# Performance work log

Measured on AMD Instinct MI355X. Metric: run time of the kernel, lower is better.

## Reference

```python
import jax, jax.numpy as jnp
import numpy as np

B, H, L, D = 2, 16, 2048, 64


def setup_inputs() -> dict:
    key = jax.random.key(0)
    kq, kk, kv = jax.random.split(key, 3)
    q = jax.random.normal(kq, (B, H, L, D), dtype=jnp.float32)
    k = jax.random.normal(kk, (B, H, L, D), dtype=jnp.float32)
    v = jax.random.normal(kv, (B, H, L, D), dtype=jnp.float32)
    return {"q": q, "k": k, "v": v}


def reference(q, k, v):
    use_norm = True
    seq_len = q.shape[-2]
    scale = q.shape[-1] ** (-0.5)
    q = q * scale
    # [B, H, L, L] score matrix
    attn = jnp.einsum("bhqd,bhkd->bhqk", q, k)
    # 2nd-order Taylor expansion of exp: 1 + s + 0.5*s^2
    attn = 1.0 + attn + 0.5 * attn * attn
    # causal mask (lower-triangular kept)
    causal = jnp.tril(jnp.ones((seq_len, seq_len), dtype=bool))
    attn = jnp.where(causal, attn, 0.0)
    o = jnp.einsum("bhqk,bhkd->bhqd", attn, v)
    if use_norm:
        z = attn.sum(-1)
        o = o / (z[..., None] + 1e-06)
    return o
```

## Files before the change

### kernel.cpp

```cpp
#include <hip/hip_runtime.h>
#include <hip/hip_bf16.h>

typedef __bf16    bf16x8  __attribute__((ext_vector_type(8)));
typedef __bf16    bf16x4  __attribute__((ext_vector_type(4)));
typedef _Float16  half8   __attribute__((ext_vector_type(8)));
typedef _Float16  half4   __attribute__((ext_vector_type(4)));
typedef _Float16  half2   __attribute__((ext_vector_type(2)));
typedef float     floatx4 __attribute__((ext_vector_type(4)));

constexpr int Bc  = 2;
constexpr int Hc  = 16;
constexpr int Lc  = 2048;
constexpr int Dc  = 64;
constexpr int BHn = Bc * Hc;
constexpr int BM  = 128;
constexpr int BN  = 128;
constexpr int NQT = Lc / BM;
constexpr int LDK = 72;
constexpr int LDV = 136;

static __device__ __forceinline__ half2 pack_f16(float a, float b) {
    return __builtin_bit_cast(half2, __builtin_amdgcn_cvt_pkrtz(a, b));
}

__global__ void prep(const float* __restrict__ kp, const float* __restrict__ vp,
                     __bf16* __restrict__ k16, _Float16* __restrict__ v16) {
    const int bid = blockIdx.x, tid = threadIdx.x;
    if (bid < 1024) {
        const size_t base = (size_t)bid * 4096 + tid * 4;
        #pragma unroll
        for (int rep = 0; rep < 4; ++rep) {
            const size_t i = base + rep * 1024;
            floatx4 v = *(const floatx4*)(kp + i);
            bf16x4 b;
            b[0] = (__bf16)v[0]; b[1] = (__bf16)v[1]; b[2] = (__bf16)v[2]; b[3] = (__bf16)v[3];
            *(bf16x4*)(k16 + i) = b;
        }
    } else {
        const int vb  = bid - 1024;
        const int bh  = vb >> 5, kt = vb & 31;
        const int key = kt * 64 + (tid & 63);
        const int k5  = key & 31;
        const int pcol = (key & ~31) | (((k5 >> 2) & 3) * 8 + ((k5 >> 4) & 1) * 4 + (k5 & 3));
        const int d0  = (tid >> 6) * 16;
        const float* src = vp + ((size_t)bh * Lc + key) * Dc;
        _Float16*    dst = v16 + (size_t)bh * Dc * Lc + pcol;
        #pragma unroll
        for (int i = 0; i < 16; ++i) {
            const int d = d0 + i;
            dst[(size_t)d * Lc] = (_Float16)src[d];
        }
    }
}

__global__ __launch_bounds__(256, 2)
void taylor_attn(const float* __restrict__ qp, const __bf16* __restrict__ k16,
                 const _Float16* __restrict__ v16, float* __restrict__ op)
{
    __shared__ __bf16   Ks[BN * LDK];
    __shared__ _Float16 VT[Dc * LDV];

    const int tid  = threadIdx.x;
    const int wv   = tid >> 6;
    const int lane = tid & 63;
    const int lm   = lane & 15;
    const int quad = lane >> 4;

    const int cu    = (int)(blockIdx.x & 255);
    const int snd   = (int)(blockIdx.x >> 8);
    const int bh    = cu & 31;
    const int qslot = cu >> 5;
    const int qi    = snd ? qslot : (NQT - 1 - qslot);
    const int q0    = qi * BM;
    const int jmax  = qi;

    const float*    qbase = qp  + ((size_t)bh * Lc + q0) * Dc;
    const __bf16*   kj    = k16 + (size_t)bh * Lc * Dc;
    const _Float16* vj    = v16 + (size_t)bh * Dc * Lc;

    bf16x8 kr[4]; half8 vr[4];
    #pragma unroll
    for (int rep = 0; rep < 4; ++rep)
        kr[rep] = *(const bf16x8*)(kj + 8 * (tid + 256 * rep));
    #pragma unroll
    for (int rep = 0; rep < 4; ++rep) {
        const int g = tid + 256 * rep;
        vr[rep] = *(const half8*)(vj + (size_t)(g >> 4) * Lc + (g & 15) * 8);
    }

    {
        const int r0 = tid >> 4, c4 = tid & 15;
        #pragma unroll
        for (int rep = 0; rep < 8; ++rep) {
            const int row = r0 + rep * 16;
            floatx4 v = *(const floatx4*)(qbase + row * Dc + c4 * 4);
            bf16x4 b;
            b[0] = (__bf16)v[0]; b[1] = (__bf16)v[1]; b[2] = (__bf16)v[2]; b[3] = (__bf16)v[3];
            *(bf16x4*)&Ks[row * LDK + c4 * 4] = b;
        }
    }
    __syncthreads();
    bf16x8 qa[2][2];
    #pragma unroll
    for (int st = 0; st < 2; ++st)
        #pragma unroll
        for (int kf = 0; kf < 2; ++kf)
            qa[st][kf] = *(const bf16x8*)&Ks[(32 * wv + 16 * st + lm) * LDK + kf * 32 + quad * 8];
    __syncthreads();

    floatx4 oacc[2][4] = {};
    floatx4 zacc[2]    = {};

    const half8 ones = {(_Float16)1.f, (_Float16)1.f, (_Float16)1.f, (_Float16)1.f,
                        (_Float16)1.f, (_Float16)1.f, (_Float16)1.f, (_Float16)1.f};
    const half2 c8  = {(_Float16)0.125f, (_Float16)0.125f};
    const half2 c1  = {(_Float16)1.f,    (_Float16)1.f};
    const half2 ch  = {(_Float16)0.5f,   (_Float16)0.5f};

    for (int j = 0; j <= jmax; ++j) {
        #pragma unroll
        for (int rep = 0; rep < 4; ++rep) {
            const int c = tid + 256 * rep;
            *(bf16x8*)&Ks[(c >> 3) * LDK + (c & 7) * 8] = kr[rep];
        }
        #pragma unroll
        for (int rep = 0; rep < 4; ++rep) {
            const int g = tid + 256 * rep;
            *(half8*)&VT[(g >> 4) * LDV + (g & 15) * 8] = vr[rep];
        }
        __syncthreads();

        if (j < jmax) {
            kj += BN * Dc;
            vj += BN;
            #pragma unroll
            for (int rep = 0; rep < 4; ++rep)
                kr[rep] = *(const bf16x8*)(kj + 8 * (tid + 256 * rep));
            #pragma unroll
            for (int rep = 0; rep < 4; ++rep) {
                const int g = tid + 256 * rep;
                vr[rep] = *(const half8*)(vj + (size_t)(g >> 4) * Lc + (g & 15) * 8);
            }
        }

        const bool nm = (j == jmax);
        #pragma unroll
        for (int half = 0; half < 2; ++half) {
            floatx4 sacc[2][4] = {};
            #pragma unroll
            for (int kb4 = 0; kb4 < 4; ++kb4) {
                const int kb = 4 * half + kb4;
                #pragma unroll
                for (int kf = 0; kf < 2; ++kf) {
                    bf16x8 ka = *(const bf16x8*)&Ks[(16 * kb + lm) * LDK + kf * 32 + quad * 8];
                    sacc[0][kb4] = __builtin_amdgcn_mfma_f32_16x16x32_bf16(ka, qa[0][kf], sacc[0][kb4], 0, 0, 0);
                    sacc[1][kb4] = __builtin_amdgcn_mfma_f32_16x16x32_bf16(ka, qa[1][kf], sacc[1][kb4], 0, 0, 0);
                }
            }

            half8 wf[2][2];
            #pragma unroll
            for (int st = 0; st < 2; ++st) {
                const int strip_lo = q0 + 32 * wv + 16 * st;
                const int thr = strip_lo + lm - j * BN;
                half2 wh[4][2];
                #pragma unroll
                for (int kb4 = 0; kb4 < 4; ++kb4) {
                    half2 s01 = pack_f16(sacc[st][kb4][0], sacc[st][kb4][1]);
                    half2 s23 = pack_f16(sacc[st][kb4][2], sacc[st][kb4][3]);
                    half2 a01 = s01 * c8 + c1;
                    half2 a23 = s23 * c8 + c1;
                    half2 w01 = a01 * (a01 * ch) + ch;
                    half2 w23 = a23 * (a23 * ch) + ch;
                    if (nm) {
                        const int i0 = 16 * (4 * half + kb4) + 4 * quad;
                        w01[0] = (i0 + 0 <= thr) ? w01[0] : (_Float16)0.f;
                        w01[1] = (i0 + 1 <= thr) ? w01[1] : (_Float16)0.f;
                        w23[0] = (i0 + 2 <= thr) ? w23[0] : (_Float16)0.f;
                        w23[1] = (i0 + 3 <= thr) ? w23[1] : (_Float16)0.f;
                    }
                    wh[kb4][0] = w01;
                    wh[kb4][1] = w23;
                }
                #pragma unroll
                for (int g2 = 0; g2 < 2; ++g2) {
                    half4 lo = __builtin_shufflevector(wh[2 * g2][0],     wh[2 * g2][1],     0, 1, 2, 3);
                    half4 hi = __builtin_shufflevector(wh[2 * g2 + 1][0], wh[2 * g2 + 1][1], 0, 1, 2, 3);
                    wf[st][g2] = __builtin_shufflevector(lo, hi, 0, 1, 2, 3, 4, 5, 6, 7);
                }
            }

            #pragma unroll
            for (int db = 0; db < 4; ++db)
                #pragma unroll
                for (int g2 = 0; g2 < 2; ++g2) {
                    const int grp = 2 * half + g2;
                    half8 va = *(const half8*)&VT[(16 * db + lm) * LDV + 32 * grp + 8 * quad];
                    oacc[0][db] = __builtin_amdgcn_mfma_f32_16x16x32_f16(va, wf[0][g2], oacc[0][db], 0, 0, 0);
                    oacc[1][db] = __builtin_amdgcn_mfma_f32_16x16x32_f16(va, wf[1][g2], oacc[1][db], 0, 0, 0);
                }
            #pragma unroll
            for (int g2 = 0; g2 < 2; ++g2) {
                zacc[0] = __builtin_amdgcn_mfma_f32_16x16x32_f16(ones, wf[0][g2], zacc[0], 0, 0, 0);
                zacc[1] = __builtin_amdgcn_mfma_f32_16x16x32_f16(ones, wf[1][g2], zacc[1], 0, 0, 0);
            }
        }
        __syncthreads();
    }

    #pragma unroll
    for (int st = 0; st < 2; ++st) {
        const float inv = 1.0f / (zacc[st][0] + 1e-6f);
        const int qrow = q0 + 32 * wv + 16 * st + lm;
        float* orow = op + ((size_t)bh * Lc + qrow) * Dc;
        #pragma unroll
        for (int db = 0; db < 4; ++db)
            #pragma unroll
            for (int r = 0; r < 4; ++r)
                orow[16 * db + 4 * quad + r] = oacc[st][db][r] * inv;
    }
}

extern "C" void kernel_launch(void* const* d_in, const int* in_sizes, int n_in,
                              void* d_out, int out_size, void* d_ws, size_t ws_size,
                              hipStream_t stream) {
    const float* q = (const float*)d_in[0];
    const float* k = (const float*)d_in[1];
    const float* v = (const float*)d_in[2];
    float* o = (float*)d_out;

    __bf16*   k16 = (__bf16*)d_ws;
    _Float16* v16 = (_Float16*)((char*)d_ws + (size_t)BHn * Lc * Dc * 2);

    prep<<<dim3(2048), dim3(256), 0, stream>>>(k, v, k16, v16);
    taylor_attn<<<dim3(NQT * BHn), dim3(256), 0, stream>>>(q, k16, v16, o);
}
```

Baseline: 119.2 us.

## Split each query tile's KV range across two blocks with atomic-flag reduction

Each query tile's causal KV loop is split into two halves handled by separate blocks, doubling the grid to 1024 blocks and rebalancing work so long diagonal tiles no longer dominate the tail. The block that finishes first writes partial O and z to workspace and sets a release flag. The second block spins on the flag, adds the partials and normalizes. Launch bounds are raised to 4 blocks per CU to fit the larger grid. The change adds workspace traffic and a spin-wait, which risks deadlock if the partner block cannot be co-resident.

```diff
diff --git a/kernel.cpp b/kernel.cpp
--- a/kernel.cpp
+++ b/kernel.cpp
@@ -24,8 +24,13 @@
 }
 
 __global__ void prep(const float* __restrict__ kp, const float* __restrict__ vp,
-                     __bf16* __restrict__ k16, _Float16* __restrict__ v16) {
+                     __bf16* __restrict__ k16, _Float16* __restrict__ v16,
+                     int* __restrict__ ctrflag) {
     const int bid = blockIdx.x, tid = threadIdx.x;
+    if (bid == 0 && tid < 256) {
+        #pragma unroll
+        for (int r = 0; r < 4; ++r) ctrflag[tid + 256 * r] = 0;
+    }
     if (bid < 1024) {
         const size_t base = (size_t)bid * 4096 + tid * 4;
         #pragma unroll
@@ -53,12 +58,15 @@
     }
 }
 
-__global__ __launch_bounds__(256, 2)
+__global__ __launch_bounds__(256, 4)
 void taylor_attn(const float* __restrict__ qp, const __bf16* __restrict__ k16,
-                 const _Float16* __restrict__ v16, float* __restrict__ op)
+                 const _Float16* __restrict__ v16, float* __restrict__ op,
+                 float* __restrict__ Oa, float* __restrict__ za,
+                 int* __restrict__ ctr, int* __restrict__ flag)
 {
     __shared__ __bf16   Ks[BN * LDK];
     __shared__ _Float16 VT[Dc * LDV];
+    __shared__ int      s_old;
 
     const int tid  = threadIdx.x;
     const int wv   = tid >> 6;
@@ -66,17 +74,20 @@
     const int lm   = lane & 15;
     const int quad = lane >> 4;
 
-    const int cu    = (int)(blockIdx.x & 255);
-    const int snd   = (int)(blockIdx.x >> 8);
-    const int bh    = cu & 31;
-    const int qslot = cu >> 5;
-    const int qi    = snd ? qslot : (NQT - 1 - qslot);
-    const int q0    = qi * BM;
-    const int jmax  = qi;
+    const int r    = (int)(blockIdx.x >> 8);
+    const int s    = (int)((blockIdx.x >> 5) & 7);
+    const int bh   = (int)(blockIdx.x & 31);
+    const int seff = (r & 1) ? (7 - s) : s;
+    const int qi   = (15 - 4 * r) - (seff >> 1);
+    const int half = seff & 1;
+    const int q0   = qi * BM;
+    const int nlo  = (qi + 2) >> 1;
+    const int j0   = half ? nlo : 0;
+    const int jend = half ? (qi + 1) : nlo;
 
     const float*    qbase = qp  + ((size_t)bh * Lc + q0) * Dc;
-    const __bf16*   kj    = k16 + (size_t)bh * Lc * Dc;
-    const _Float16* vj    = v16 + (size_t)bh * Dc * Lc;
+    const __bf16*   kj    = k16 + (size_t)bh * Lc * Dc + (size_t)j0 * BN * Dc;
+    const _Float16* vj    = v16 + (size_t)bh * Dc * Lc + (size_t)j0 * BN;
 
     bf16x8 kr[4]; half8 vr[4];
     #pragma unroll
@@ -117,7 +128,7 @@
     const half2 c1  = {(_Float16)1.f,    (_Float16)1.f};
     const half2 ch  = {(_Float16)0.5f,   (_Float16)0.5f};
 
-    for (int j = 0; j <= jmax; ++j) {
+    for (int j = j0; j < jend; ++j) {
         #pragma unroll
         for (int rep = 0; rep < 4; ++rep) {
             const int c = tid + 256 * rep;
@@ -130,7 +141,7 @@
         }
         __syncthreads();
 
-        if (j < jmax) {
+        if (j + 1 < jend) {
             kj += BN * Dc;
             vj += BN;
             #pragma unroll
@@ -143,13 +154,13 @@
             }
         }
 
-        const bool nm = (j == jmax);
-        #pragma unroll
-        for (int half = 0; half < 2; ++half) {
+        const bool nm = (j == qi);
+        #pragma unroll
+        for (int kh = 0; kh < 2; ++kh) {
             floatx4 sacc[2][4] = {};
             #pragma unroll
             for (int kb4 = 0; kb4 < 4; ++kb4) {
-                const int kb = 4 * half + kb4;
+                const int kb = 4 * kh + kb4;
                 #pragma unroll
                 for (int kf = 0; kf < 2; ++kf) {
                     bf16x8 ka = *(const bf16x8*)&Ks[(16 * kb + lm) * LDK + kf * 32 + quad * 8];
@@ -173,7 +184,7 @@
                     half2 w01 = a01 * (a01 * ch) + ch;
                     half2 w23 = a23 * (a23 * ch) + ch;
                     if (nm) {
-                        const int i0 = 16 * (4 * half + kb4) + 4 * quad;
+                        const int i0 = 16 * (4 * kh + kb4) + 4 * quad;
                         w01[0] = (i0 + 0 <= thr) ? w01[0] : (_Float16)0.f;
                         w01[1] = (i0 + 1 <= thr) ? w01[1] : (_Float16)0.f;
                         w23[0] = (i0 + 2 <= thr) ? w23[0] : (_Float16)0.f;
@@ -194,7 +205,7 @@
             for (int db = 0; db < 4; ++db)
                 #pragma unroll
                 for (int g2 = 0; g2 < 2; ++g2) {
-                    const int grp = 2 * half + g2;
+                    const int grp = 2 * kh + g2;
                     half8 va = *(const half8*)&VT[(16 * db + lm) * LDV + 32 * grp + 8 * quad];
                     oacc[0][db] = __builtin_amdgcn_mfma_f32_16x16x32_f16(va, wf[0][g2], oacc[0][db], 0, 0, 0);
                     oacc[1][db] = __builtin_amdgcn_mfma_f32_16x16x32_f16(va, wf[1][g2], oacc[1][db], 0, 0, 0);
@@ -208,16 +219,55 @@
         __syncthreads();
     }
 
+    const int pid = (qi << 5) | bh;
+    float* Opart = Oa + (size_t)pid * (256 * 32);
+    float* zpart = za + (size_t)pid * 128;
+
+    if (tid == 0) s_old = atomicAdd(&ctr[pid], 1);
+    __syncthreads();
+
+    if (s_old == 0) {
+        float* dst = Opart + tid * 32;
+        #pragma unroll
+        for (int st = 0; st < 2; ++st)
+            #pragma unroll
+            for (int db = 0; db < 4; ++db)
+                *(floatx4*)(dst + (st * 4 + db) * 4) = oacc[st][db];
+        if (quad == 0) {
+            zpart[32 * wv + lm]      = zacc[0][0];
+            zpart[32 * wv + 16 + lm] = zacc[1][0];
+        }
+        __threadfence();
+        __syncthreads();
+        if (tid == 0)
+            __hip_atomic_store(&flag[pid], 1, __ATOMIC_RELEASE, __HIP_MEMORY_SCOPE_AGENT);
+        return;
+    }
+
+    if (tid == 0) {
+        while (__hip_atomic_load(&flag[pid], __ATOMIC_ACQUIRE, __HIP_MEMORY_SCOPE_AGENT) == 0) {}
+    }
+    __syncthreads();
+    __threadfence();
+
+    const float* src = Opart + tid * 32;
+    #pragma unroll
+    for (int st = 0; st < 2; ++st)
+        #pragma unroll
+        for (int db = 0; db < 4; ++db)
+            oacc[st][db] += *(const floatx4*)(src + (st * 4 + db) * 4);
+    const float zo[2] = {zpart[32 * wv + lm], zpart[32 * wv + 16 + lm]};
+
     #pragma unroll
     for (int st = 0; st < 2; ++st) {
-        const float inv = 1.0f / (zacc[st][0] + 1e-6f);
+        const float inv = 1.0f / (zacc[st][0] + zo[st] + 1e-6f);
         const int qrow = q0 + 32 * wv + 16 * st + lm;
         float* orow = op + ((size_t)bh * Lc + qrow) * Dc;
         #pragma unroll
         for (int db = 0; db < 4; ++db)
             #pragma unroll
-            for (int r = 0; r < 4; ++r)
-                orow[16 * db + 4 * quad + r] = oacc[st][db][r] * inv;
+            for (int rr = 0; rr < 4; ++rr)
+                orow[16 * db + 4 * quad + rr] = oacc[st][db][rr] * inv;
     }
 }
 
@@ -229,9 +279,16 @@
     const float* v = (const float*)d_in[2];
     float* o = (float*)d_out;
 
-    __bf16*   k16 = (__bf16*)d_ws;
-    _Float16* v16 = (_Float16*)((char*)d_ws + (size_t)BHn * Lc * Dc * 2);
-
-    prep<<<dim3(2048), dim3(256), 0, stream>>>(k, v, k16, v16);
-    taylor_attn<<<dim3(NQT * BHn), dim3(256), 0, stream>>>(q, k16, v16, o);
-}
+    char* ws = (char*)d_ws;
+    constexpr size_t SZ_KV = (size_t)BHn * Lc * Dc * 2;
+    constexpr size_t SZ_OA = (size_t)512 * 256 * 32 * 4;
+    constexpr size_t SZ_ZA = (size_t)512 * 128 * 4;
+    __bf16*   k16 = (__bf16*)ws;
+    _Float16* v16 = (_Float16*)(ws + SZ_KV);
+    float*    Oa  = (float*)(ws + 2 * SZ_KV);
+    float*    za  = (float*)(ws + 2 * SZ_KV + SZ_OA);
+    int*      ctf = (int*)(ws + 2 * SZ_KV + SZ_OA + SZ_ZA);
+
+    prep<<<dim3(2048), dim3(256), 0, stream>>>(k, v, k16, v16, ctf);
+    taylor_attn<<<dim3(1024), dim3(256), 0, stream>>>(q, k16, v16, o, Oa, za, ctf, ctf + 512);
+}
```

Result: slower. 358.4 us (+200.5%).
